# Kernel tuning notes

Measured on AMD Instinct MI355X. Metric: run time of the kernel, lower is better.

## Reference

```python
import jax, jax.numpy as jnp
import numpy as np

NGROUP, CIN, COUT, K, HIDDEN = 8, 16, 16, 5, True


def _build_mask():
    # Group-causal PixelCNN-style mask for a 5x5 kernel.
    # Spatial: rows above center fully visible; center row visible left of center.
    # Center tap: input group g_in visible to output group g_out iff
    #   g_in <= g_out (hidden layer) or g_in < g_out (input layer).
    nout, cinall = NGROUP * COUT, NGROUP * CIN
    c = K // 2
    m = np.zeros((nout, cinall, K, K), dtype=np.float32)
    m[:, :, :c, :] = 1.0          # rows strictly above center
    m[:, :, c, :c] = 1.0          # center row, left of center
    g_out = np.arange(nout)[:, None] // COUT   # (nout,1)
    g_in = np.arange(cinall)[None, :] // CIN   # (1,cinall)
    center_ok = (g_in <= g_out) if HIDDEN else (g_in < g_out)
    m[:, :, c, c] = center_ok.astype(np.float32)
    return jnp.asarray(m)

_MASK = _build_mask()


def setup_inputs() -> dict:
    key = jax.random.key(0)
    k1, k2 = jax.random.split(key)
    x = jax.random.normal(k1, (8, 128, 256, 512), dtype=jnp.float32)
    weight = jax.random.uniform(k2, (128, 128, 5, 5), dtype=jnp.float32)
    bias = jnp.zeros((128,), dtype=jnp.float32)
    slope = jnp.zeros((128,), dtype=jnp.float32)  # PReLU slope (zero -> ReLU)
    return {"x": x, "weight": weight, "bias": bias, "slope": slope}


def reference(x, weight, bias, slope):
    w = weight * _MASK  # apply causal group mask
    # context pad by 2 then valid 5x5 conv == SAME padding conv
    y = jax.lax.conv_general_dilated(
        x, w, window_strides=(1, 1), padding=((2, 2), (2, 2)),
        dimension_numbers=("NCHW", "OIHW", "NCHW"))
    y = y + bias[None, :, None, None]
    a = slope[None, :, None, None]
    return jnp.where(y > 0, y, a * y)  # per-channel PReLU
```

## Files before the change

kernel.cpp:

```cpp
#include <hip/hip_runtime.h>
#include <hip/hip_bf16.h>

typedef __attribute__((ext_vector_type(8))) short short8;
typedef __attribute__((ext_vector_type(4))) float f32x4;

#define CH 128
#define H 256
#define W 512
#define PH 258
#define PW 516
#define NTAPS 13
#define P_BYTES (PH * PW * CH * 2)

#define GRAN_PER_ROW 544
#define BUF_GRAN 2304
#define BUF_SHORTS (BUF_GRAN * 8)
#define ROW_SHORTS (136 * 32)

#define GLD_LDS16(g, l)                                                        \
  __builtin_amdgcn_global_load_lds(                                            \
      (const __attribute__((address_space(1))) void*)(g),                      \
      (__attribute__((address_space(3))) void*)(l), 16, 0, 0)

__global__ void premask_weights(const float* __restrict__ w,
                                __hip_bfloat16* __restrict__ Wt2) {
    int idx  = blockIdx.x * 256 + threadIdx.x;
    int frag = idx >> 9;
    int r    = idx & 511;
    int l    = r >> 3;
    int e    = r & 7;
    int t    = frag >> 5;
    int ob   = (frag >> 2) & 7;
    int kcg  = frag & 3;
    int oc   = ob * 16 + (l & 15);
    int ic   = kcg * 32 + (l >> 4) * 8 + e;
    int ky   = t < 5 ? 0 : (t < 10 ? 1 : 2);
    int kx   = t - ky * 5;
    float v  = w[(oc * CH + ic) * 25 + ky * 5 + kx];
    if (t == 12 && ((ic >> 4) > (oc >> 4))) v = 0.f;
    Wt2[idx] = __float2bfloat16(v);
}

__global__ void transpose_pad_kernel(const float* __restrict__ xn,
                                     __hip_bfloat16* __restrict__ P) {
    __shared__ float tile[32][33];
    int h  = blockIdx.y;
    int wt = blockIdx.x & 15;
    int ct = blockIdx.x >> 4;
    int tx = threadIdx.x & 31;
    int ty = threadIdx.x >> 5;
#pragma unroll
    for (int r = 0; r < 4; ++r) {
        int c = ct * 32 + ty + r * 8;
        tile[ty + r * 8][tx] = xn[(c * H + h) * W + wt * 32 + tx];
    }
    __syncthreads();
    int wl = threadIdx.x >> 3;
    int cq = threadIdx.x & 7;
    union { ushort4 u; __hip_bfloat16 h[4]; } v;
    v.h[0] = __float2bfloat16(tile[cq * 4 + 0][wl]);
    v.h[1] = __float2bfloat16(tile[cq * 4 + 1][wl]);
    v.h[2] = __float2bfloat16(tile[cq * 4 + 2][wl]);
    v.h[3] = __float2bfloat16(tile[cq * 4 + 3][wl]);
    *reinterpret_cast<ushort4*>(
        (unsigned short*)P +
        ((size_t)(h + 2) * PW + (wt * 32 + wl + 2)) * CH + ct * 32 + cq * 4) = v.u;
}

__global__ __launch_bounds__(256, 2)
void conv_mfma(const __hip_bfloat16* __restrict__ P,
               const __hip_bfloat16* __restrict__ Wt2,
               const float* __restrict__ bias,
               const float* __restrict__ slope,
               float* __restrict__ outn) {
    __shared__ short lds[2 * BUF_SHORTS];
    int h0    = blockIdx.y << 1;
    int w0    = blockIdx.x << 7;
    int tid   = threadIdx.x;
    int lane  = tid & 63;
    int wv    = tid >> 6;
    int l15   = lane & 15;
    int khi   = lane >> 4;
    int obf   = (wv >> 1) * 4;
    int hsel  = wv & 1;

    f32x4 acc[4][8];
#pragma unroll
    for (int mi = 0; mi < 4; ++mi)
#pragma unroll
        for (int ni = 0; ni < 8; ++ni)
            acc[mi][ni] = (f32x4){0.f, 0.f, 0.f, 0.f};

    const short* Wt2s = (const short*)Wt2;

    int stoff[9];
#pragma unroll
    for (int i = 0; i < 9; ++i) {
        int s    = wv + i * 4;
        int g64  = (s << 6) + lane;
        int row  = (g64 >= 544) + (g64 >= 1088) + (g64 >= 1632) + (g64 >= 2176);
        int rem  = g64 - row * GRAN_PER_ROW;
        int px   = rem >> 2;
        int chk  = rem & 3;
        int rowc = row < 4 ? row : 3;
        int pxc  = px < 132 ? px : 131;
        int ccs  = chk ^ (px & 3);
        stoff[i] = ((h0 + rowc) * PW + (w0 + pxc)) * CH + ccs * 8;
    }
    int bq[5];
#pragma unroll
    for (int kx = 0; kx < 5; ++kx) {
        int pxb = kx + l15;
        bq[kx] = (pxb * 4 + (khi ^ (pxb & 3))) * 8;
    }

    auto stage = [&](int kk, int b) {
#pragma unroll
        for (int i = 0; i < 9; ++i)
            GLD_LDS16(P + stoff[i] + kk * 32,
                      (char*)lds + b * (BUF_SHORTS * 2) + ((wv + i * 4) << 10));
    };

    stage(0, 0);
    __syncthreads();

    for (int kk = 0; kk < 4; ++kk) {
        int cur = kk & 1;
        if (kk < 3) stage(kk + 1, cur ^ 1);

        const short* apb = Wt2s + ((obf * 4 + kk) << 9) + (lane << 3);
        const short* bb  = lds + cur * BUF_SHORTS + hsel * ROW_SHORTS;
#pragma unroll
        for (int t = 0; t < NTAPS; ++t) {
            int ky  = t < 5 ? 0 : (t < 10 ? 1 : 2);
            int kx  = t - ky * 5;
            const short* ap = apb + t * 16384;
            const short* bp = bb + ky * ROW_SHORTS + bq[kx];
            short8 a[4], b[8];
#pragma unroll
            for (int mi = 0; mi < 4; ++mi)
                a[mi] = *reinterpret_cast<const short8*>(ap + mi * 2048);
#pragma unroll
            for (int ni = 0; ni < 8; ++ni)
                b[ni] = *reinterpret_cast<const short8*>(bp + ni * 512);
            __builtin_amdgcn_s_setprio(1);
#pragma unroll
            for (int mi = 0; mi < 4; ++mi)
#pragma unroll
                for (int ni = 0; ni < 8; ++ni)
                    acc[mi][ni] = __builtin_amdgcn_mfma_f32_16x16x32_bf16(
                        a[mi], b[ni], acc[mi][ni], 0, 0, 0);
            __builtin_amdgcn_s_setprio(0);
        }
        __syncthreads();
    }

    int hrow = h0 + hsel;
#pragma unroll
    for (int mi = 0; mi < 4; ++mi) {
        int ocb = obf * 16 + mi * 16 + 4 * khi;
        f32x4 b4 = *reinterpret_cast<const f32x4*>(bias + ocb);
        f32x4 s4 = *reinterpret_cast<const f32x4*>(slope + ocb);
#pragma unroll
        for (int i = 0; i < 4; ++i) {
            float* orow = outn + ((ocb + i) * H + hrow) * W + w0;
#pragma unroll
            for (int ni = 0; ni < 8; ++ni) {
                float v = acc[mi][ni][i] + b4[i];
                v = v > 0.f ? v : s4[i] * v;
                orow[ni * 16 + l15] = v;
            }
        }
    }
}

extern "C" void kernel_launch(void* const* d_in, const int* in_sizes, int n_in,
                              void* d_out, int out_size, void* d_ws, size_t ws_size,
                              hipStream_t stream) {
    const float* x      = (const float*)d_in[0];
    const float* weight = (const float*)d_in[1];
    const float* bias   = (const float*)d_in[2];
    const float* slope  = (const float*)d_in[3];
    float* out = (float*)d_out;

    __hip_bfloat16* P   = (__hip_bfloat16*)d_ws;
    __hip_bfloat16* Wt2 = (__hip_bfloat16*)((char*)d_ws + P_BYTES);

    (void)hipMemsetAsync(d_ws, 0, P_BYTES, stream);
    premask_weights<<<832, 256, 0, stream>>>(weight, Wt2);

    for (int n = 0; n < 8; ++n) {
        const float* xn = x + (size_t)n * CH * H * W;
        float* on       = out + (size_t)n * CH * H * W;
        transpose_pad_kernel<<<dim3(64, 256), 256, 0, stream>>>(xn, P);
        conv_mfma<<<dim3(4, 128), 256, 0, stream>>>(P, Wt2, bias, slope, on);
    }
}
```

Measured before the change: 650.9 us.

## Switch conv to 32x32x16 MFMA and fuse next-batch transpose into conv epilogue

The conv kernel moves from 16x16x32 to 32x32x16 bf16 MFMA tiles, with a new weight fragment layout and new LDS B-fragment addressing, so fewer operand loads are needed per FLOP. The per-batch transpose/pad kernel is also folded into the tail of the conv kernel: each block converts a slice of the next batch into a second, double-buffered padded buffer. This removes separate launches and lets the transpose overlap with conv tails. The cost is a doubled workspace, extra memset, and a serial transpose loop appended to each block.

```diff
diff --git a/kernel.cpp b/kernel.cpp
--- a/kernel.cpp
+++ b/kernel.cpp
@@ -3,6 +3,7 @@
 
 typedef __attribute__((ext_vector_type(8))) short short8;
 typedef __attribute__((ext_vector_type(4))) float f32x4;
+typedef __attribute__((ext_vector_type(16))) float f32x16;
 
 #define CH 128
 #define H 256
@@ -11,6 +12,7 @@
 #define PW 516
 #define NTAPS 13
 #define P_BYTES (PH * PW * CH * 2)
+#define CHW (CH * H * W)
 
 #define GRAN_PER_ROW 544
 #define BUF_GRAN 2304
@@ -23,22 +25,23 @@
       (__attribute__((address_space(3))) void*)(l), 16, 0, 0)
 
 __global__ void premask_weights(const float* __restrict__ w,
-                                __hip_bfloat16* __restrict__ Wt2) {
+                                __hip_bfloat16* __restrict__ Wt3) {
     int idx  = blockIdx.x * 256 + threadIdx.x;
     int frag = idx >> 9;
     int r    = idx & 511;
     int l    = r >> 3;
     int e    = r & 7;
     int t    = frag >> 5;
-    int ob   = (frag >> 2) & 7;
-    int kcg  = frag & 3;
-    int oc   = ob * 16 + (l & 15);
-    int ic   = kcg * 32 + (l >> 4) * 8 + e;
+    int mib  = (frag >> 3) & 3;
+    int kk   = (frag >> 1) & 3;
+    int ks   = frag & 1;
+    int oc   = mib * 32 + (l & 31);
+    int ic   = kk * 32 + ks * 16 + (l >> 5) * 8 + e;
     int ky   = t < 5 ? 0 : (t < 10 ? 1 : 2);
     int kx   = t - ky * 5;
     float v  = w[(oc * CH + ic) * 25 + ky * 5 + kx];
     if (t == 12 && ((ic >> 4) > (oc >> 4))) v = 0.f;
-    Wt2[idx] = __float2bfloat16(v);
+    Wt3[idx] = __float2bfloat16(v);
 }
 
 __global__ void transpose_pad_kernel(const float* __restrict__ xn,
@@ -57,11 +60,11 @@
     __syncthreads();
     int wl = threadIdx.x >> 3;
     int cq = threadIdx.x & 7;
-    union { ushort4 u; __hip_bfloat16 h[4]; } v;
-    v.h[0] = __float2bfloat16(tile[cq * 4 + 0][wl]);
-    v.h[1] = __float2bfloat16(tile[cq * 4 + 1][wl]);
-    v.h[2] = __float2bfloat16(tile[cq * 4 + 2][wl]);
-    v.h[3] = __float2bfloat16(tile[cq * 4 + 3][wl]);
+    union { ushort4 u; __hip_bfloat16 hh[4]; } v;
+    v.hh[0] = __float2bfloat16(tile[cq * 4 + 0][wl]);
+    v.hh[1] = __float2bfloat16(tile[cq * 4 + 1][wl]);
+    v.hh[2] = __float2bfloat16(tile[cq * 4 + 2][wl]);
+    v.hh[3] = __float2bfloat16(tile[cq * 4 + 3][wl]);
     *reinterpret_cast<ushort4*>(
         (unsigned short*)P +
         ((size_t)(h + 2) * PW + (wt * 32 + wl + 2)) * CH + ct * 32 + cq * 4) = v.u;
@@ -69,29 +72,31 @@
 
 __global__ __launch_bounds__(256, 2)
 void conv_mfma(const __hip_bfloat16* __restrict__ P,
-               const __hip_bfloat16* __restrict__ Wt2,
+               const __hip_bfloat16* __restrict__ Wt3,
                const float* __restrict__ bias,
                const float* __restrict__ slope,
-               float* __restrict__ outn) {
+               float* __restrict__ outn,
+               const float* __restrict__ xnext,
+               __hip_bfloat16* __restrict__ Pnext) {
     __shared__ short lds[2 * BUF_SHORTS];
     int h0    = blockIdx.y << 1;
     int w0    = blockIdx.x << 7;
     int tid   = threadIdx.x;
     int lane  = tid & 63;
     int wv    = tid >> 6;
-    int l15   = lane & 15;
-    int khi   = lane >> 4;
-    int obf   = (wv >> 1) * 4;
+    int l31   = lane & 31;
+    int lhi   = lane >> 5;
+    int obf2  = wv >> 1;
     int hsel  = wv & 1;
 
-    f32x4 acc[4][8];
-#pragma unroll
-    for (int mi = 0; mi < 4; ++mi)
-#pragma unroll
-        for (int ni = 0; ni < 8; ++ni)
-            acc[mi][ni] = (f32x4){0.f, 0.f, 0.f, 0.f};
-
-    const short* Wt2s = (const short*)Wt2;
+    f32x16 acc[2][4];
+#pragma unroll
+    for (int mi = 0; mi < 2; ++mi)
+#pragma unroll
+        for (int ni = 0; ni < 4; ++ni)
+            acc[mi][ni] = (f32x16){0.f};
+
+    const short* Wt3s = (const short*)Wt3;
 
     int stoff[9];
 #pragma unroll
@@ -107,11 +112,13 @@
         int ccs  = chk ^ (px & 3);
         stoff[i] = ((h0 + rowc) * PW + (w0 + pxc)) * CH + ccs * 8;
     }
-    int bq[5];
+    int bqk[5][2];
 #pragma unroll
     for (int kx = 0; kx < 5; ++kx) {
-        int pxb = kx + l15;
-        bq[kx] = (pxb * 4 + (khi ^ (pxb & 3))) * 8;
+        int pxb = kx + l31;
+#pragma unroll
+        for (int ks = 0; ks < 2; ++ks)
+            bqk[kx][ks] = (pxb * 4 + ((ks * 2 + lhi) ^ (pxb & 3))) * 8;
     }
 
     auto stage = [&](int kk, int b) {
@@ -128,28 +135,36 @@
         int cur = kk & 1;
         if (kk < 3) stage(kk + 1, cur ^ 1);
 
-        const short* apb = Wt2s + ((obf * 4 + kk) << 9) + (lane << 3);
-        const short* bb  = lds + cur * BUF_SHORTS + hsel * ROW_SHORTS;
+        const short* apb = Wt3s + obf2 * 8192 + kk * 1024 + (lane << 3);
+        const short* bb  = lds + cur * BUF_SHORTS;
 #pragma unroll
         for (int t = 0; t < NTAPS; ++t) {
             int ky  = t < 5 ? 0 : (t < 10 ? 1 : 2);
             int kx  = t - ky * 5;
             const short* ap = apb + t * 16384;
-            const short* bp = bb + ky * ROW_SHORTS + bq[kx];
-            short8 a[4], b[8];
-#pragma unroll
-            for (int mi = 0; mi < 4; ++mi)
-                a[mi] = *reinterpret_cast<const short8*>(ap + mi * 2048);
-#pragma unroll
-            for (int ni = 0; ni < 8; ++ni)
-                b[ni] = *reinterpret_cast<const short8*>(bp + ni * 512);
+            const short* bp = bb + (hsel + ky) * ROW_SHORTS;
+            short8 a[2][2], b[4][2];
+#pragma unroll
+            for (int mi = 0; mi < 2; ++mi)
+#pragma unroll
+                for (int ks = 0; ks < 2; ++ks)
+                    a[mi][ks] = *reinterpret_cast<const short8*>(
+                        ap + mi * 4096 + ks * 512);
+#pragma unroll
+            for (int ni = 0; ni < 4; ++ni)
+#pragma unroll
+                for (int ks = 0; ks < 2; ++ks)
+                    b[ni][ks] = *reinterpret_cast<const short8*>(
+                        bp + bqk[kx][ks] + ni * 1024);
             __builtin_amdgcn_s_setprio(1);
 #pragma unroll
-            for (int mi = 0; mi < 4; ++mi)
-#pragma unroll
-                for (int ni = 0; ni < 8; ++ni)
-                    acc[mi][ni] = __builtin_amdgcn_mfma_f32_16x16x32_bf16(
-                        a[mi], b[ni], acc[mi][ni], 0, 0, 0);
+            for (int mi = 0; mi < 2; ++mi)
+#pragma unroll
+                for (int ni = 0; ni < 4; ++ni)
+#pragma unroll
+                    for (int ks = 0; ks < 2; ++ks)
+                        acc[mi][ni] = __builtin_amdgcn_mfma_f32_32x32x16_bf16(
+                            a[mi][ks], b[ni][ks], acc[mi][ni], 0, 0, 0);
             __builtin_amdgcn_s_setprio(0);
         }
         __syncthreads();
@@ -157,19 +172,53 @@
 
     int hrow = h0 + hsel;
 #pragma unroll
-    for (int mi = 0; mi < 4; ++mi) {
-        int ocb = obf * 16 + mi * 16 + 4 * khi;
-        f32x4 b4 = *reinterpret_cast<const f32x4*>(bias + ocb);
-        f32x4 s4 = *reinterpret_cast<const f32x4*>(slope + ocb);
-#pragma unroll
-        for (int i = 0; i < 4; ++i) {
-            float* orow = outn + ((ocb + i) * H + hrow) * W + w0;
-#pragma unroll
-            for (int ni = 0; ni < 8; ++ni) {
-                float v = acc[mi][ni][i] + b4[i];
-                v = v > 0.f ? v : s4[i] * v;
-                orow[ni * 16 + l15] = v;
+    for (int mi = 0; mi < 2; ++mi) {
+#pragma unroll
+        for (int q = 0; q < 4; ++q) {
+            int oc0 = obf2 * 64 + mi * 32 + q * 8 + 4 * lhi;
+            f32x4 b4 = *reinterpret_cast<const f32x4*>(bias + oc0);
+            f32x4 s4 = *reinterpret_cast<const f32x4*>(slope + oc0);
+#pragma unroll
+            for (int j = 0; j < 4; ++j) {
+                float* orow = outn + ((oc0 + j) * H + hrow) * W + w0;
+#pragma unroll
+                for (int ni = 0; ni < 4; ++ni) {
+                    float v = acc[mi][ni][q * 4 + j] + b4[j];
+                    v = v > 0.f ? v : s4[j] * v;
+                    orow[ni * 32 + l31] = v;
+                }
             }
+        }
+    }
+
+    if (xnext) {
+        float* sc = (float*)lds;
+        int cb = blockIdx.y * 4 + blockIdx.x;
+        int tx = tid & 31;
+        int ty = tid >> 5;
+        int wl = tid >> 3;
+        int cq = tid & 7;
+        for (int i = 0; i < 32; ++i) {
+            int vt  = cb * 32 + i;
+            int hh  = vt >> 6;
+            int vbx = vt & 63;
+            int wt  = vbx & 15;
+            int ct  = vbx >> 4;
+            __syncthreads();
+#pragma unroll
+            for (int r = 0; r < 4; ++r) {
+                int c = ct * 32 + ty + r * 8;
+                sc[(ty + r * 8) * 33 + tx] = xnext[(c * H + hh) * W + wt * 32 + tx];
+            }
+            __syncthreads();
+            union { ushort4 u; __hip_bfloat16 hh4[4]; } v;
+            v.hh4[0] = __float2bfloat16(sc[(cq * 4 + 0) * 33 + wl]);
+            v.hh4[1] = __float2bfloat16(sc[(cq * 4 + 1) * 33 + wl]);
+            v.hh4[2] = __float2bfloat16(sc[(cq * 4 + 2) * 33 + wl]);
+            v.hh4[3] = __float2bfloat16(sc[(cq * 4 + 3) * 33 + wl]);
+            *reinterpret_cast<ushort4*>(
+                (unsigned short*)Pnext +
+                ((size_t)(hh + 2) * PW + (wt * 32 + wl + 2)) * CH + ct * 32 + cq * 4) = v.u;
         }
     }
 }
@@ -183,16 +232,19 @@
     const float* slope  = (const float*)d_in[3];
     float* out = (float*)d_out;
 
-    __hip_bfloat16* P   = (__hip_bfloat16*)d_ws;
-    __hip_bfloat16* Wt2 = (__hip_bfloat16*)((char*)d_ws + P_BYTES);
-
-    (void)hipMemsetAsync(d_ws, 0, P_BYTES, stream);
-    premask_weights<<<832, 256, 0, stream>>>(weight, Wt2);
+    __hip_bfloat16* P0  = (__hip_bfloat16*)d_ws;
+    __hip_bfloat16* P1  = (__hip_bfloat16*)((char*)d_ws + P_BYTES);
+    __hip_bfloat16* Wt3 = (__hip_bfloat16*)((char*)d_ws + 2 * (size_t)P_BYTES);
+    __hip_bfloat16* Pp[2] = {P0, P1};
+
+    (void)hipMemsetAsync(d_ws, 0, 2 * (size_t)P_BYTES, stream);
+    premask_weights<<<832, 256, 0, stream>>>(weight, Wt3);
+    transpose_pad_kernel<<<dim3(64, 256), 256, 0, stream>>>(x, P0);
 
     for (int n = 0; n < 8; ++n) {
-        const float* xn = x + (size_t)n * CH * H * W;
-        float* on       = out + (size_t)n * CH * H * W;
-        transpose_pad_kernel<<<dim3(64, 256), 256, 0, stream>>>(xn, P);
-        conv_mfma<<<dim3(4, 128), 256, 0, stream>>>(P, Wt2, bias, slope, on);
-    }
-}
+        const float* xnext = (n < 7) ? x + (size_t)(n + 1) * CHW : nullptr;
+        conv_mfma<<<dim3(4, 128), 256, 0, stream>>>(
+            Pp[n & 1], Wt3, bias, slope, out + (size_t)n * CHW,
+            xnext, Pp[(n + 1) & 1]);
+    }
+}
```

New measurement: 766.0 us. 17.7% more time.

## Batch all images into single launches and enlarge conv tile to four rows

Applied to the files above, without the earlier changes.

Replaces the per-image loop of transpose and conv launches with single batched launches over all eight images, using a per-image padded workspace. The full workspace memset is replaced by a kernel that zeroes only the pad border. The conv kernel moves to 512 threads covering four output rows, so each staged halo of six input rows is shared by more outputs and the halo overhead per output row drops. In exchange the workspace grows eightfold, LDS use per block rises, and register pressure under the new launch bounds may limit occupancy.

```diff
diff --git a/kernel.cpp b/kernel.cpp
--- a/kernel.cpp
+++ b/kernel.cpp
@@ -11,16 +11,33 @@
 #define PW 516
 #define NTAPS 13
 #define P_BYTES (PH * PW * CH * 2)
+#define P_SHORTS (PH * PW * CH)
+#define CHW (CH * H * W)
 
 #define GRAN_PER_ROW 544
-#define BUF_GRAN 2304
-#define BUF_SHORTS (BUF_GRAN * 8)
+#define NLOADS 52
+#define BUF_SHORTS (3328 * 8)
 #define ROW_SHORTS (136 * 32)
 
 #define GLD_LDS16(g, l)                                                        \
   __builtin_amdgcn_global_load_lds(                                            \
       (const __attribute__((address_space(1))) void*)(g),                      \
       (__attribute__((address_space(3))) void*)(l), 16, 0, 0)
+
+__global__ void zero_pads(unsigned int* __restrict__ Pd) {
+    int row  = blockIdx.x;
+    int slab = blockIdx.y;
+    unsigned int* base = Pd + (size_t)slab * (P_SHORTS / 2);
+    int tid = threadIdx.x;
+    if (row < 2) {
+        unsigned int* r = base + (size_t)row * (PW * 64);
+        for (int i = tid; i < PW * 64; i += 256) r[i] = 0u;
+    } else {
+        int seg = tid >> 6;
+        int col = seg < 2 ? seg : 512 + seg;
+        base[((size_t)row * PW + col) * 64 + (tid & 63)] = 0u;
+    }
+}
 
 __global__ void premask_weights(const float* __restrict__ w,
                                 __hip_bfloat16* __restrict__ Wt2) {
@@ -41,9 +58,11 @@
     Wt2[idx] = __float2bfloat16(v);
 }
 
-__global__ void transpose_pad_kernel(const float* __restrict__ xn,
-                                     __hip_bfloat16* __restrict__ P) {
+__global__ void transpose_pad_all(const float* __restrict__ x,
+                                  __hip_bfloat16* __restrict__ Pbase) {
     __shared__ float tile[32][33];
+    const float* xn = x + (size_t)blockIdx.z * CHW;
+    unsigned short* P = (unsigned short*)(Pbase + (size_t)blockIdx.z * P_SHORTS);
     int h  = blockIdx.y;
     int wt = blockIdx.x & 15;
     int ct = blockIdx.x >> 4;
@@ -57,32 +76,33 @@
     __syncthreads();
     int wl = threadIdx.x >> 3;
     int cq = threadIdx.x & 7;
-    union { ushort4 u; __hip_bfloat16 h[4]; } v;
-    v.h[0] = __float2bfloat16(tile[cq * 4 + 0][wl]);
-    v.h[1] = __float2bfloat16(tile[cq * 4 + 1][wl]);
-    v.h[2] = __float2bfloat16(tile[cq * 4 + 2][wl]);
-    v.h[3] = __float2bfloat16(tile[cq * 4 + 3][wl]);
+    union { ushort4 u; __hip_bfloat16 hh[4]; } v;
+    v.hh[0] = __float2bfloat16(tile[cq * 4 + 0][wl]);
+    v.hh[1] = __float2bfloat16(tile[cq * 4 + 1][wl]);
+    v.hh[2] = __float2bfloat16(tile[cq * 4 + 2][wl]);
+    v.hh[3] = __float2bfloat16(tile[cq * 4 + 3][wl]);
     *reinterpret_cast<ushort4*>(
-        (unsigned short*)P +
-        ((size_t)(h + 2) * PW + (wt * 32 + wl + 2)) * CH + ct * 32 + cq * 4) = v.u;
-}
-
-__global__ __launch_bounds__(256, 2)
-void conv_mfma(const __hip_bfloat16* __restrict__ P,
-               const __hip_bfloat16* __restrict__ Wt2,
-               const float* __restrict__ bias,
-               const float* __restrict__ slope,
-               float* __restrict__ outn) {
+        P + ((size_t)(h + 2) * PW + (wt * 32 + wl + 2)) * CH + ct * 32 + cq * 4) = v.u;
+}
+
+__global__ __launch_bounds__(512, 2)
+void conv_mfma_all(const __hip_bfloat16* __restrict__ Pbase,
+                   const __hip_bfloat16* __restrict__ Wt2,
+                   const float* __restrict__ bias,
+                   const float* __restrict__ slope,
+                   float* __restrict__ out) {
     __shared__ short lds[2 * BUF_SHORTS];
-    int h0    = blockIdx.y << 1;
+    const __hip_bfloat16* P = Pbase + (size_t)blockIdx.z * P_SHORTS;
+    float* outn = out + (size_t)blockIdx.z * CHW;
+    int h0    = blockIdx.y << 2;
     int w0    = blockIdx.x << 7;
     int tid   = threadIdx.x;
     int lane  = tid & 63;
     int wv    = tid >> 6;
     int l15   = lane & 15;
     int khi   = lane >> 4;
-    int obf   = (wv >> 1) * 4;
-    int hsel  = wv & 1;
+    int obf   = (wv & 1) * 4;
+    int hsel  = wv >> 1;
 
     f32x4 acc[4][8];
 #pragma unroll
@@ -93,19 +113,19 @@
 
     const short* Wt2s = (const short*)Wt2;
 
-    int stoff[9];
-#pragma unroll
-    for (int i = 0; i < 9; ++i) {
-        int s    = wv + i * 4;
+    int stoff[7];
+#pragma unroll
+    for (int i = 0; i < 7; ++i) {
+        int s    = wv + i * 8;
         int g64  = (s << 6) + lane;
-        int row  = (g64 >= 544) + (g64 >= 1088) + (g64 >= 1632) + (g64 >= 2176);
+        int row  = (g64 >= 544) + (g64 >= 1088) + (g64 >= 1632) +
+                   (g64 >= 2176) + (g64 >= 2720);
         int rem  = g64 - row * GRAN_PER_ROW;
         int px   = rem >> 2;
         int chk  = rem & 3;
-        int rowc = row < 4 ? row : 3;
         int pxc  = px < 132 ? px : 131;
-        int ccs  = chk ^ (px & 3);
-        stoff[i] = ((h0 + rowc) * PW + (w0 + pxc)) * CH + ccs * 8;
+        int ccs  = chk ^ (pxc & 3);
+        stoff[i] = ((h0 + row) * PW + (w0 + pxc)) * CH + ccs * 8;
     }
     int bq[5];
 #pragma unroll
@@ -116,9 +136,12 @@
 
     auto stage = [&](int kk, int b) {
 #pragma unroll
-        for (int i = 0; i < 9; ++i)
-            GLD_LDS16(P + stoff[i] + kk * 32,
-                      (char*)lds + b * (BUF_SHORTS * 2) + ((wv + i * 4) << 10));
+        for (int i = 0; i < 7; ++i) {
+            int s = wv + i * 8;
+            if (s < NLOADS)
+                GLD_LDS16(P + stoff[i] + kk * 32,
+                          (char*)lds + b * (BUF_SHORTS * 2) + (s << 10));
+        }
     };
 
     stage(0, 0);
@@ -183,16 +206,11 @@
     const float* slope  = (const float*)d_in[3];
     float* out = (float*)d_out;
 
-    __hip_bfloat16* P   = (__hip_bfloat16*)d_ws;
-    __hip_bfloat16* Wt2 = (__hip_bfloat16*)((char*)d_ws + P_BYTES);
-
-    (void)hipMemsetAsync(d_ws, 0, P_BYTES, stream);
+    __hip_bfloat16* Pbase = (__hip_bfloat16*)d_ws;
+    __hip_bfloat16* Wt2   = (__hip_bfloat16*)((char*)d_ws + 8 * (size_t)P_BYTES);
+
+    zero_pads<<<dim3(PH, 8), 256, 0, stream>>>((unsigned int*)d_ws);
     premask_weights<<<832, 256, 0, stream>>>(weight, Wt2);
-
-    for (int n = 0; n < 8; ++n) {
-        const float* xn = x + (size_t)n * CH * H * W;
-        float* on       = out + (size_t)n * CH * H * W;
-        transpose_pad_kernel<<<dim3(64, 256), 256, 0, stream>>>(xn, P);
-        conv_mfma<<<dim3(4, 128), 256, 0, stream>>>(P, Wt2, bias, slope, on);
-    }
-}
+    transpose_pad_all<<<dim3(64, 256, 8), 256, 0, stream>>>(x, Pbase);
+    conv_mfma_all<<<dim3(4, 64, 8), 512, 0, stream>>>(Pbase, Wt2, bias, slope, out);
+}
```

After: 592.0 us. -9.0%, faster.
